# Kernel optimization log

Hardware: AMD Instinct MI355X
Metric: run time of the kernel (lower is better)

The kernel has to match this reference:

```python
import jax, jax.numpy as jnp
import numpy as np

N, E, IN, HID = 8192, 8192, 256, 256
DEG_P = 0.004  # avg degree ~32


def setup_inputs() -> dict:
    key = jax.random.key(0)
    ks = jax.random.split(key, 16)
    x = jax.random.normal(ks[0], (N, IN), dtype=jnp.float32)
    adj = (jax.random.uniform(ks[1], (N, N)) < DEG_P).astype(jnp.float32)
    tar_ei = jax.random.randint(ks[2], (2, E), 0, N, dtype=jnp.int32)
    s = 0.05
    return {
        'x': x, 'adj': adj, 'tar_ei': tar_ei,
        'W1c': jax.random.normal(ks[3], (IN, HID)) * s, 'b1c': jnp.zeros((HID,)),
        'W2c': jax.random.normal(ks[4], (HID, HID)) * s, 'b2c': jnp.zeros((HID,)),
        'W1j': jax.random.normal(ks[5], (IN, HID)) * s, 'b1j': jnp.zeros((HID,)),
        'W2j': jax.random.normal(ks[6], (HID, HID)) * s, 'b2j': jnp.zeros((HID,)),
        'Wl1': jax.random.normal(ks[7], (HID, HID)) * s, 'bl1': jnp.zeros((HID,)),
        'Wl2': jax.random.normal(ks[8], (HID, HID)) * s, 'bl2': jnp.zeros((HID,)),
        'Wout': jax.random.normal(ks[9], (HID, 1)) * s, 'bout': jnp.zeros((1,)),
    }


def _mlp2(h, W1, b1, W2, b2):
    # Linear -> ReLU -> (Dropout: eval-mode identity) -> Linear
    return jax.nn.relu(h @ W1 + b1) @ W2 + b2


def reference(x, adj, tar_ei, W1c, b1c, W2c, b2c, W1j, b1j, W2j, b2j,
              Wl1, bl1, Wl2, bl2, Wout, bout):
    beta = 1.0
    xi = x[tar_ei[0]]            # [E, IN]
    xj = x[tar_ei[1]]            # [E, IN]
    ai = adj[tar_ei[0]]          # [E, N] gathered adjacency rows
    aj = adj[tar_ei[1]]          # [E, N]
    # common-neighbor overlap + spmm_add aggregation: cn = ai*aj; xcn = cn @ x
    xcn = (ai * aj) @ x          # [E, IN]
    xij = _mlp2(xi * xj, W1j, b1j, W2j, b2j)
    xcn = _mlp2(xcn, W1c, b1c, W2c, b2c)
    h = beta * xcn + xij
    h = jax.nn.relu(h @ Wl1 + bl1)
    h = jax.nn.relu(h @ Wl2 + bl2)
    out = h @ Wout + bout        # [E, 1]
    return out.squeeze()
```

## Files before the change

### kernel.cpp

```cpp
#include <hip/hip_runtime.h>
#include <stdint.h>

#define NN 8192
#define NE 8192
#define DIM 256
#define NW 128
#define HCAP 64
#define TE 32

typedef short bf16x8 __attribute__((ext_vector_type(8)));
typedef float f32x4 __attribute__((ext_vector_type(4)));

__device__ __forceinline__ unsigned short f2bf(float f) {
  uint32_t u = __builtin_bit_cast(uint32_t, f);
  u += 0x7fffu + ((u >> 16) & 1u);
  return (unsigned short)(u >> 16);
}
__device__ __forceinline__ float bf2f(unsigned short h) {
  uint32_t u = ((uint32_t)h) << 16;
  return __builtin_bit_cast(float, u);
}

__global__ __launch_bounds__(256) void prep_kernel(
    const float* __restrict__ adj,
    const float* __restrict__ W1c, const float* __restrict__ W2c,
    const float* __restrict__ W1j, const float* __restrict__ W2j,
    const float* __restrict__ Wl1, const float* __restrict__ Wl2,
    unsigned short* __restrict__ Wt,
    unsigned long long* __restrict__ bits) {
  const int blk = blockIdx.x;
  if (blk < 1536) {
    const float* Ws[6] = {W1c, W2c, W1j, W2j, Wl1, Wl2};
    const int w = blk >> 8;
    const int n = blk & 255;
    const int k = threadIdx.x;
    Wt[w * 65536 + n * DIM + k] = f2bf(Ws[w][k * DIM + n]);
  } else {
    const float4* __restrict__ adjv = (const float4*)adj;
    const int lane = threadIdx.x & 63;
    const int wv = (blk - 1536) * 4 + (threadIdx.x >> 6);
    const int nwv = 4096 * 4;
    const int total = NN * 32;
    for (int t = 2 * wv; t < total; t += 2 * nwv) {
      const int t1 = t + 1;
      float4 v0 = adjv[(size_t)(t >> 5) * 2048 + (t & 31) * 64 + lane];
      float4 v1 = adjv[(size_t)(t1 >> 5) * 2048 + (t1 & 31) * 64 + lane];
      unsigned long long m0 = __ballot(v0.x != 0.0f);
      unsigned long long m1 = __ballot(v0.y != 0.0f);
      unsigned long long m2 = __ballot(v0.z != 0.0f);
      unsigned long long m3 = __ballot(v0.w != 0.0f);
      unsigned long long n0 = __ballot(v1.x != 0.0f);
      unsigned long long n1 = __ballot(v1.y != 0.0f);
      unsigned long long n2 = __ballot(v1.z != 0.0f);
      unsigned long long n3 = __ballot(v1.w != 0.0f);
      if (lane == 0) {
        unsigned long long* p0 = bits + (size_t)(t >> 5) * NW + (t & 31) * 4;
        unsigned long long* p1 = bits + (size_t)(t1 >> 5) * NW + (t1 & 31) * 4;
        p0[0] = m0; p0[1] = m1; p0[2] = m2; p0[3] = m3;
        p1[0] = n0; p1[1] = n1; p1[2] = n2; p1[3] = n3;
      }
    }
  }
}


#define LDP 264

__device__ __forceinline__ void load_w(const unsigned short* __restrict__ Wt,
                                       bf16x8 w[2][8], int lane, int wave) {
  const int lr = lane & 15;
  const int kl = (lane >> 4) * 8;
  const int n0 = wave * 32;
#pragma unroll
  for (int kk = 0; kk < 8; ++kk) {
    const int k0 = kk * 32 + kl;
    w[0][kk] = *(const bf16x8*)(Wt + (size_t)(n0 + lr) * DIM + k0);
    w[1][kk] = *(const bf16x8*)(Wt + (size_t)(n0 + 16 + lr) * DIM + k0);
  }
}

__device__ __forceinline__ void gemm_reg(const unsigned short (*src)[LDP],
                                         const bf16x8 w[2][8],
                                         f32x4 acc[2][2], int lane) {
  const int lr = lane & 15;
  const int kl = (lane >> 4) * 8;
#pragma unroll
  for (int kk = 0; kk < 8; ++kk) {
    const int k0 = kk * 32 + kl;
    bf16x8 a0 = *(const bf16x8*)(&src[lr][k0]);
    bf16x8 a1 = *(const bf16x8*)(&src[16 + lr][k0]);
    acc[0][0] = __builtin_amdgcn_mfma_f32_16x16x32_bf16(a0, w[0][kk], acc[0][0], 0, 0, 0);
    acc[0][1] = __builtin_amdgcn_mfma_f32_16x16x32_bf16(a0, w[1][kk], acc[0][1], 0, 0, 0);
    acc[1][0] = __builtin_amdgcn_mfma_f32_16x16x32_bf16(a1, w[0][kk], acc[1][0], 0, 0, 0);
    acc[1][1] = __builtin_amdgcn_mfma_f32_16x16x32_bf16(a1, w[1][kk], acc[1][1], 0, 0, 0);
  }
}

__device__ __forceinline__ void zero22(f32x4 a[2][2]) {
#pragma unroll
  for (int m = 0; m < 2; ++m)
#pragma unroll
    for (int n = 0; n < 2; ++n) {
      f32x4 z = {0.f, 0.f, 0.f, 0.f};
      a[m][n] = z;
    }
}

__device__ __forceinline__ void epilogue32(f32x4 acc[2][2], float bb0, float bb1,
                                           bool relu, unsigned short (*dst)[LDP],
                                           int lane, int wave) {
  const int lc = lane & 15;
  const int rg = (lane >> 4) * 4;
#pragma unroll
  for (int n = 0; n < 2; ++n) {
    const int col = wave * 32 + n * 16 + lc;
    const float bb = n ? bb1 : bb0;
#pragma unroll
    for (int m = 0; m < 2; ++m)
#pragma unroll
      for (int q = 0; q < 4; ++q) {
        float v = acc[m][n][q] + bb;
        if (relu) v = fmaxf(v, 0.f);
        dst[m * 16 + rg + q][col] = f2bf(v);
      }
  }
}

__global__ __launch_bounds__(512, 2) void fused_kernel(
    const float* __restrict__ x,
    const unsigned long long* __restrict__ bits,
    const int* __restrict__ tar,
    const unsigned short* __restrict__ Wt,
    const float* __restrict__ b1c, const float* __restrict__ b2c,
    const float* __restrict__ b1j, const float* __restrict__ b2j,
    const float* __restrict__ bl1, const float* __restrict__ bl2,
    const float* __restrict__ Wout, const float* __restrict__ bout,
    float* __restrict__ out) {
  __shared__ unsigned short lA[TE][LDP];
  __shared__ unsigned short lB[TE][LDP];
  __shared__ unsigned short lC[TE][LDP];
  __shared__ int hits[TE][HCAP];
  __shared__ int nh[TE];

  const int tid = threadIdx.x;
  const int lane = tid & 63;
  const int wave = tid >> 6;
  const int e0 = blockIdx.x * TE;

  const int lc = lane & 15;
  const int c0 = wave * 32 + lc;
  const int c1 = c0 + 16;
  const float vb1c0 = b1c[c0], vb1c1 = b1c[c1];
  const float vb1j0 = b1j[c0], vb1j1 = b1j[c1];
  const float vb20 = b2c[c0] + b2j[c0], vb21 = b2c[c1] + b2j[c1];
  const float vbl10 = bl1[c0], vbl11 = bl1[c1];
  const float vbl20 = bl2[c0], vbl21 = bl2[c1];
  const int gpart = tid & 15;
  float wv[16];
#pragma unroll
  for (int q = 0; q < 16; ++q) wv[q] = Wout[gpart * 16 + q];
  const float vbout = bout[0];

  if (tid < TE) nh[tid] = 0;

  const int e_a = tid >> 4;
  const int t16 = tid & 15;
  const int ia = tar[e0 + e_a];
  const int ja = tar[NE + e0 + e_a];
  unsigned long long bw_i[8], bw_j[8];
  {
    const unsigned long long* bi = bits + (size_t)ia * NW + t16 * 8;
    const unsigned long long* bj = bits + (size_t)ja * NW + t16 * 8;
#pragma unroll
    for (int q = 0; q < 8; ++q) { bw_i[q] = bi[q]; bw_j[q] = bj[q]; }
  }

  {
    const int col = tid & 255;
    const int sub = tid >> 8;
    float vi[16], vj[16];
#pragma unroll
    for (int p = 0; p < 16; ++p) {
      const int e = sub * 16 + p;
      vi[p] = x[(size_t)tar[e0 + e] * DIM + col];
      vj[p] = x[(size_t)tar[NE + e0 + e] * DIM + col];
    }
#pragma unroll
    for (int p = 0; p < 16; ++p)
      lC[sub * 16 + p][col] = f2bf(vi[p] * vj[p]);
  }
  __syncthreads();

#pragma unroll
  for (int q = 0; q < 8; ++q) {
    unsigned long long m = bw_i[q] & bw_j[q];
    const int w = t16 * 8 + q;
    const int base = (w >> 2) << 8;
    const int qq = w & 3;
    while (m) {
      int b = __builtin_ctzll(m);
      m &= m - 1;
      int idx = atomicAdd(&nh[e_a], 1);
      if (idx < HCAP) hits[e_a][idx] = base + (b << 2) + qq;
    }
  }
  __syncthreads();

  bf16x8 wX[2][8], wY[2][8];
  load_w(Wt + 0 * 65536, wX, lane, wave);
  load_w(Wt + 1 * 65536, wY, lane, wave);
  {
    const int col = tid & 255;
    const int sub = tid >> 8;
#pragma unroll
    for (int p = 0; p < 16; ++p) {
      const int e = sub * 16 + p;
      const int n = nh[e] < HCAP ? nh[e] : HCAP;
      float xc = 0.f;
      for (int h = 0; h < n; ++h)
        xc += x[(size_t)hits[e][h] * DIM + col];
      lA[e][col] = f2bf(xc);
    }
  }
  __syncthreads();

  f32x4 acc[2][2], pAcc[2][2];

  zero22(acc);
  gemm_reg(lA, wX, acc, lane);
  load_w(Wt + 2 * 65536, wX, lane, wave);
  epilogue32(acc, vb1c0, vb1c1, true, lB, lane, wave);
  __syncthreads();

  zero22(pAcc);
  gemm_reg(lB, wY, pAcc, lane);
  load_w(Wt + 3 * 65536, wY, lane, wave);
  zero22(acc);
  gemm_reg(lC, wX, acc, lane);
  epilogue32(acc, vb1j0, vb1j1, true, lA, lane, wave);
  __syncthreads();

  gemm_reg(lA, wY, pAcc, lane);
  load_w(Wt + 4 * 65536, wX, lane, wave);
  {
    const int rg = (lane >> 4) * 4;
#pragma unroll
    for (int n = 0; n < 2; ++n) {
      const int col = wave * 32 + n * 16 + lc;
      const float bb = n ? vb21 : vb20;
#pragma unroll
      for (int m = 0; m < 2; ++m)
#pragma unroll
        for (int q = 0; q < 4; ++q)
          lB[m * 16 + rg + q][col] = f2bf(pAcc[m][n][q] + bb);
    }
  }
  __syncthreads();

  zero22(acc);
  gemm_reg(lB, wX, acc, lane);
  load_w(Wt + 5 * 65536, wY, lane, wave);
  epilogue32(acc, vbl10, vbl11, true, lA, lane, wave);
  __syncthreads();

  zero22(acc);
  gemm_reg(lA, wY, acc, lane);
  epilogue32(acc, vbl20, vbl21, true, lB, lane, wave);
  __syncthreads();

  const int el = tid >> 4;
  float s = 0.f;
#pragma unroll
  for (int q = 0; q < 16; ++q)
    s += bf2f(lB[el][gpart * 16 + q]) * wv[q];
#pragma unroll
  for (int o = 8; o; o >>= 1) s += __shfl_xor(s, o);
  if (gpart == 0) out[e0 + el] = s + vbout;
}

extern "C" void kernel_launch(void* const* d_in, const int* in_sizes, int n_in,
                              void* d_out, int out_size, void* d_ws, size_t ws_size,
                              hipStream_t stream) {
  const float* x    = (const float*)d_in[0];
  const float* adj  = (const float*)d_in[1];
  const int*   tar  = (const int*)d_in[2];
  const float* W1c  = (const float*)d_in[3];
  const float* b1c  = (const float*)d_in[4];
  const float* W2c  = (const float*)d_in[5];
  const float* b2c  = (const float*)d_in[6];
  const float* W1j  = (const float*)d_in[7];
  const float* b1j  = (const float*)d_in[8];
  const float* W2j  = (const float*)d_in[9];
  const float* b2j  = (const float*)d_in[10];
  const float* Wl1  = (const float*)d_in[11];
  const float* bl1  = (const float*)d_in[12];
  const float* Wl2  = (const float*)d_in[13];
  const float* bl2  = (const float*)d_in[14];
  const float* Wout = (const float*)d_in[15];
  const float* bout = (const float*)d_in[16];

  char* ws = (char*)d_ws;
  unsigned short*     Wt   = (unsigned short*)(ws);
  unsigned long long* bits = (unsigned long long*)(ws + (1u << 20));

  prep_kernel<<<1536 + 4096, 256, 0, stream>>>(adj, W1c, W2c, W1j, W2j, Wl1,
                                               Wl2, Wt, bits);

  fused_kernel<<<NE / TE, 512, 0, stream>>>(x, bits, tar, Wt, b1c, b2c, b1j,
                                            b2j, bl1, bl2, Wout, bout,
                                            (float*)d_out);
}
```

Measured before the change: 81.22 us.

## Merge prep and fused kernels into one cooperative kernel with grid sync

Replaces the separate prep kernel (weight transpose to bf16 and adjacency bitmask build) and the main fused kernel with a single cooperative launch of 256 blocks. Each block first does its share of the weight conversion and bitmask ballots, with software prefetch of the next adjacency rows, then a grid-wide sync, then the existing per-edge pipeline. The aim is to drop the kernel launch gap and overlap the x gathers with prep. The cost is a grid barrier, and the adjacency scan now runs on far fewer waves, which may limit memory bandwidth during prep.

```diff
diff --git a/kernel.cpp b/kernel.cpp
--- a/kernel.cpp
+++ b/kernel.cpp
@@ -1,5 +1,8 @@
 #include <hip/hip_runtime.h>
+#include <hip/hip_cooperative_groups.h>
 #include <stdint.h>
+
+namespace cg = cooperative_groups;
 
 #define NN 8192
 #define NE 8192
@@ -7,6 +10,7 @@
 #define NW 128
 #define HCAP 64
 #define TE 32
+#define NBLK 256
 
 typedef short bf16x8 __attribute__((ext_vector_type(8)));
 typedef float f32x4 __attribute__((ext_vector_type(4)));
@@ -20,49 +24,6 @@
   uint32_t u = ((uint32_t)h) << 16;
   return __builtin_bit_cast(float, u);
 }
-
-__global__ __launch_bounds__(256) void prep_kernel(
-    const float* __restrict__ adj,
-    const float* __restrict__ W1c, const float* __restrict__ W2c,
-    const float* __restrict__ W1j, const float* __restrict__ W2j,
-    const float* __restrict__ Wl1, const float* __restrict__ Wl2,
-    unsigned short* __restrict__ Wt,
-    unsigned long long* __restrict__ bits) {
-  const int blk = blockIdx.x;
-  if (blk < 1536) {
-    const float* Ws[6] = {W1c, W2c, W1j, W2j, Wl1, Wl2};
-    const int w = blk >> 8;
-    const int n = blk & 255;
-    const int k = threadIdx.x;
-    Wt[w * 65536 + n * DIM + k] = f2bf(Ws[w][k * DIM + n]);
-  } else {
-    const float4* __restrict__ adjv = (const float4*)adj;
-    const int lane = threadIdx.x & 63;
-    const int wv = (blk - 1536) * 4 + (threadIdx.x >> 6);
-    const int nwv = 4096 * 4;
-    const int total = NN * 32;
-    for (int t = 2 * wv; t < total; t += 2 * nwv) {
-      const int t1 = t + 1;
-      float4 v0 = adjv[(size_t)(t >> 5) * 2048 + (t & 31) * 64 + lane];
-      float4 v1 = adjv[(size_t)(t1 >> 5) * 2048 + (t1 & 31) * 64 + lane];
-      unsigned long long m0 = __ballot(v0.x != 0.0f);
-      unsigned long long m1 = __ballot(v0.y != 0.0f);
-      unsigned long long m2 = __ballot(v0.z != 0.0f);
-      unsigned long long m3 = __ballot(v0.w != 0.0f);
-      unsigned long long n0 = __ballot(v1.x != 0.0f);
-      unsigned long long n1 = __ballot(v1.y != 0.0f);
-      unsigned long long n2 = __ballot(v1.z != 0.0f);
-      unsigned long long n3 = __ballot(v1.w != 0.0f);
-      if (lane == 0) {
-        unsigned long long* p0 = bits + (size_t)(t >> 5) * NW + (t & 31) * 4;
-        unsigned long long* p1 = bits + (size_t)(t1 >> 5) * NW + (t1 & 31) * 4;
-        p0[0] = m0; p0[1] = m1; p0[2] = m2; p0[3] = m3;
-        p1[0] = n0; p1[1] = n1; p1[2] = n2; p1[3] = n3;
-      }
-    }
-  }
-}
-
 
 #define LDP 264
 
@@ -126,15 +87,19 @@
   }
 }
 
-__global__ __launch_bounds__(512, 2) void fused_kernel(
+__global__ __launch_bounds__(512, 2) void coop_kernel(
     const float* __restrict__ x,
-    const unsigned long long* __restrict__ bits,
+    const float* __restrict__ adj,
     const int* __restrict__ tar,
-    const unsigned short* __restrict__ Wt,
+    const float* __restrict__ W1c, const float* __restrict__ W2c,
+    const float* __restrict__ W1j, const float* __restrict__ W2j,
+    const float* __restrict__ Wl1, const float* __restrict__ Wl2,
     const float* __restrict__ b1c, const float* __restrict__ b2c,
     const float* __restrict__ b1j, const float* __restrict__ b2j,
     const float* __restrict__ bl1, const float* __restrict__ bl2,
     const float* __restrict__ Wout, const float* __restrict__ bout,
+    unsigned short* __restrict__ Wt,
+    unsigned long long* __restrict__ bits,
     float* __restrict__ out) {
   __shared__ unsigned short lA[TE][LDP];
   __shared__ unsigned short lB[TE][LDP];
@@ -145,7 +110,10 @@
   const int tid = threadIdx.x;
   const int lane = tid & 63;
   const int wave = tid >> 6;
-  const int e0 = blockIdx.x * TE;
+  const int blk = blockIdx.x;
+  const int e0 = blk * TE;
+
+  if (tid < TE) nh[tid] = 0;
 
   const int lc = lane & 15;
   const int c0 = wave * 32 + lc;
@@ -161,20 +129,6 @@
   for (int q = 0; q < 16; ++q) wv[q] = Wout[gpart * 16 + q];
   const float vbout = bout[0];
 
-  if (tid < TE) nh[tid] = 0;
-
-  const int e_a = tid >> 4;
-  const int t16 = tid & 15;
-  const int ia = tar[e0 + e_a];
-  const int ja = tar[NE + e0 + e_a];
-  unsigned long long bw_i[8], bw_j[8];
-  {
-    const unsigned long long* bi = bits + (size_t)ia * NW + t16 * 8;
-    const unsigned long long* bj = bits + (size_t)ja * NW + t16 * 8;
-#pragma unroll
-    for (int q = 0; q < 8; ++q) { bw_i[q] = bi[q]; bw_j[q] = bj[q]; }
-  }
-
   {
     const int col = tid & 255;
     const int sub = tid >> 8;
@@ -189,26 +143,80 @@
     for (int p = 0; p < 16; ++p)
       lC[sub * 16 + p][col] = f2bf(vi[p] * vj[p]);
   }
-  __syncthreads();
-
-#pragma unroll
-  for (int q = 0; q < 8; ++q) {
-    unsigned long long m = bw_i[q] & bw_j[q];
-    const int w = t16 * 8 + q;
-    const int base = (w >> 2) << 8;
-    const int qq = w & 3;
-    while (m) {
-      int b = __builtin_ctzll(m);
-      m &= m - 1;
-      int idx = atomicAdd(&nh[e_a], 1);
-      if (idx < HCAP) hits[e_a][idx] = base + (b << 2) + qq;
-    }
-  }
-  __syncthreads();
+
+  {
+    const int gid = blk * 512 + tid;
+#pragma unroll
+    for (int r = 0; r < 3; ++r) {
+      const int eid = gid + r * 131072;
+      const int w = eid >> 16;
+      const int rem = eid & 65535;
+      const int k = rem >> 8;
+      const int n = rem & 255;
+      const float* W = (w < 1) ? W1c : (w < 2) ? W2c : (w < 3) ? W1j
+                     : (w < 4) ? W2j : (w < 5) ? Wl1 : Wl2;
+      Wt[w * 65536 + n * DIM + k] = f2bf(W[rem]);
+    }
+  }
+
+  {
+    const float4* __restrict__ adjv = (const float4*)adj;
+    const int base = blk * 1024;
+    int tt = wave * 2;
+    float4 v0 = adjv[(size_t)((base + tt) >> 5) * 2048 + ((base + tt) & 31) * 64 + lane];
+    float4 v1 = adjv[(size_t)((base + tt + 1) >> 5) * 2048 + ((base + tt + 1) & 31) * 64 + lane];
+    for (; tt < 1024; tt += 16) {
+      const int t = base + tt;
+      const int tn = (tt + 16 < 1024) ? base + tt + 16 : base;
+      float4 p0v = adjv[(size_t)(tn >> 5) * 2048 + (tn & 31) * 64 + lane];
+      float4 p1v = adjv[(size_t)((tn + 1) >> 5) * 2048 + ((tn + 1) & 31) * 64 + lane];
+      unsigned long long m0 = __ballot(v0.x != 0.0f);
+      unsigned long long m1 = __ballot(v0.y != 0.0f);
+      unsigned long long m2 = __ballot(v0.z != 0.0f);
+      unsigned long long m3 = __ballot(v0.w != 0.0f);
+      unsigned long long k0 = __ballot(v1.x != 0.0f);
+      unsigned long long k1 = __ballot(v1.y != 0.0f);
+      unsigned long long k2 = __ballot(v1.z != 0.0f);
+      unsigned long long k3 = __ballot(v1.w != 0.0f);
+      if (lane == 0) {
+        unsigned long long* p0 = bits + (size_t)(t >> 5) * NW + (t & 31) * 4;
+        unsigned long long* p1 = bits + (size_t)((t + 1) >> 5) * NW + ((t + 1) & 31) * 4;
+        p0[0] = m0; p0[1] = m1; p0[2] = m2; p0[3] = m3;
+        p1[0] = k0; p1[1] = k1; p1[2] = k2; p1[3] = k3;
+      }
+      v0 = p0v; v1 = p1v;
+    }
+  }
+
+  cg::this_grid().sync();
 
   bf16x8 wX[2][8], wY[2][8];
   load_w(Wt + 0 * 65536, wX, lane, wave);
   load_w(Wt + 1 * 65536, wY, lane, wave);
+
+  {
+    const int e_a = tid >> 4;
+    const int t16 = tid & 15;
+    const int ia = tar[e0 + e_a];
+    const int ja = tar[NE + e0 + e_a];
+    const unsigned long long* bi = bits + (size_t)ia * NW + t16 * 8;
+    const unsigned long long* bj = bits + (size_t)ja * NW + t16 * 8;
+#pragma unroll
+    for (int q = 0; q < 8; ++q) {
+      unsigned long long m = bi[q] & bj[q];
+      const int w = t16 * 8 + q;
+      const int base = (w >> 2) << 8;
+      const int qq = w & 3;
+      while (m) {
+        int b = __builtin_ctzll(m);
+        m &= m - 1;
+        int idx = atomicAdd(&nh[e_a], 1);
+        if (idx < HCAP) hits[e_a][idx] = base + (b << 2) + qq;
+      }
+    }
+  }
+  __syncthreads();
+
   {
     const int col = tid & 255;
     const int sub = tid >> 8;
@@ -302,11 +310,16 @@
   char* ws = (char*)d_ws;
   unsigned short*     Wt   = (unsigned short*)(ws);
   unsigned long long* bits = (unsigned long long*)(ws + (1u << 20));
-
-  prep_kernel<<<1536 + 4096, 256, 0, stream>>>(adj, W1c, W2c, W1j, W2j, Wl1,
-                                               Wl2, Wt, bits);
-
-  fused_kernel<<<NE / TE, 512, 0, stream>>>(x, bits, tar, Wt, b1c, b2c, b1j,
-                                            b2j, bl1, bl2, Wout, bout,
-                                            (float*)d_out);
-}
+  float* out = (float*)d_out;
+
+  void* args[] = {
+      (void*)&x, (void*)&adj, (void*)&tar,
+      (void*)&W1c, (void*)&W2c, (void*)&W1j, (void*)&W2j,
+      (void*)&Wl1, (void*)&Wl2,
+      (void*)&b1c, (void*)&b2c, (void*)&b1j, (void*)&b2j,
+      (void*)&bl1, (void*)&bl2, (void*)&Wout, (void*)&bout,
+      (void*)&Wt, (void*)&bits, (void*)&out};
+
+  hipLaunchCooperativeKernel((const void*)coop_kernel, dim3(NBLK), dim3(512),
+                             args, 0, stream);
+}
```

Result: slower. 143.5 us (+76.7%).
